# Performance work log

Hardware: AMD Instinct MI355X
Metric: run time of the kernel (lower is better)

## Reference

```python
import jax, jax.numpy as jnp
from jax import lax
import numpy as np

DN = ('NCHW', 'OIHW', 'NCHW')


def conv(x, w, b, pad=0):
    y = lax.conv_general_dilated(x, w, (1, 1), [(pad, pad), (pad, pad)],
                                 dimension_numbers=DN)
    return y + b[None, :, None, None]


def deconv(x, w, b, stride=1):
    # PyTorch ConvTranspose2d weight is (in, out, kH, kW); equivalent conv uses
    # flipped, in/out-transposed kernel with lhs dilation = stride, pad = k-1.
    k = w.shape[2]
    wt = jnp.flip(w, (2, 3)).transpose(1, 0, 2, 3)
    y = lax.conv_general_dilated(x, wt, (1, 1), [(k - 1, k - 1), (k - 1, k - 1)],
                                 lhs_dilation=(stride, stride), dimension_numbers=DN)
    return y + b[None, :, None, None]


def maxpool2(x):
    return lax.reduce_window(x, -jnp.inf, lax.max, (1, 1, 2, 2), (1, 1, 2, 2), 'VALID')


def setup_inputs() -> dict:
    key = jax.random.key(0)
    ks = jax.random.split(key, 12)
    B = 256

    def he(k, shape, fan_in):
        return jax.random.normal(k, shape, jnp.float32) * np.sqrt(2.0 / fan_in)

    inp = {
        'x': jax.random.normal(ks[0], (B, 1, 28, 28), jnp.float32),
        # encoder convs
        'w1': he(ks[1], (128, 1, 5, 5), 1 * 25), 'b1': jnp.zeros((128,), jnp.float32),
        'w2': he(ks[2], (128, 128, 5, 5), 128 * 25), 'b2': jnp.zeros((128,), jnp.float32),
        'w3': he(ks[3], (128, 128, 5, 5), 128 * 25), 'b3': jnp.zeros((128,), jnp.float32),
        # decoder transposed convs (torch shape: in, out, kH, kW)
        't1w': he(ks[4], (128, 128, 4, 4), 128 * 16), 't1b': jnp.zeros((128,), jnp.float32),
        't2w': he(ks[5], (128, 128, 4, 4), 128 * 16), 't2b': jnp.zeros((128,), jnp.float32),
        't3w': he(ks[6], (128, 128, 5, 5), 128 * 25), 't3b': jnp.zeros((128,), jnp.float32),
        't4w': he(ks[7], (128, 128, 5, 5), 128 * 25), 't4b': jnp.zeros((128,), jnp.float32),
        # mu_net 1x1 conv
        'mw': he(ks[8], (1, 128, 1, 1), 128), 'mb': jnp.zeros((1,), jnp.float32),
        # codebook: Embedding(128, 128), init ~ N(0, 1)
        'dict_w': jax.random.normal(ks[9], (128, 128), jnp.float32),
    }
    return inp


def reference(x, w1, b1, w2, b2, w3, b3,
              t1w, t1b, t2w, t2b, t3w, t3b, t4w, t4b,
              mw, mb, dict_w):
    BETA, RATE = 0.25, 5.0
    # ---- encoder ----
    h = jax.nn.relu(conv(x, w1, b1, pad=0))          # (B,128,24,24)
    h = jax.nn.relu(conv(h, w2, b2, pad=2))          # (B,128,24,24)
    h = maxpool2(h)                                  # (B,128,12,12)
    h = conv(h, w3, b3, pad=2)                       # (B,128,12,12)
    z = maxpool2(h)                                  # (B,128,6,6)

    # ---- nearest_neighbor (faithful: argmax of distance, as in the source) ----
    z_sg = lax.stop_gradient(z)
    z2 = jnp.sum(z_sg * z_sg, axis=1, keepdims=True)          # (B,1,6,6)
    w2n = jnp.sum(dict_w * dict_w, axis=1)                     # (K,)
    cross = jnp.einsum('bchw,kc->bkhw', z_sg, lax.stop_gradient(dict_w))
    d2 = z2 + w2n[None, :, None, None] - 2.0 * cross           # (B,K,6,6)
    index = jnp.argmax(d2, axis=1)                             # (B,6,6) int

    # ---- embedding gather ----
    val = dict_w[index].transpose(0, 3, 1, 2)                  # (B,128,6,6)

    # ---- decoder on detached codes ----
    f = lax.stop_gradient(val)
    f = jax.nn.relu(deconv(f, t1w, t1b, stride=1))             # (B,128,9,9)
    f = jax.nn.relu(deconv(f, t2w, t2b, stride=2))             # (B,128,20,20)
    f = jax.nn.relu(deconv(f, t3w, t3b, stride=1))             # (B,128,24,24)
    f = jax.nn.relu(deconv(f, t4w, t4b, stride=1))             # (B,128,28,28)
    mu = conv(f, mw, mb, pad=0)                                # (B,1,28,28)

    loss_rec = jnp.mean((mu - x) ** 2)
    dict_loss = jnp.mean((val - lax.stop_gradient(z)) ** 2) * RATE
    enc_loss = jnp.mean((z - lax.stop_gradient(val)) ** 2) * BETA * RATE
    var_loss = jnp.zeros((), jnp.float32)
    losses = jnp.stack([loss_rec, dict_loss, enc_loss, var_loss])
    return losses, index
```

## Files before the change

### kernel.cpp

```cpp
#include <hip/hip_runtime.h>
#include <hip/hip_bf16.h>


#define B_ 256

typedef __attribute__((ext_vector_type(8))) short s16x8;
typedef __attribute__((ext_vector_type(4))) short s16x4;
typedef __attribute__((ext_vector_type(8))) _Float16 f16x8;
typedef __attribute__((ext_vector_type(4))) float f32x4;

__device__ inline ushort f2bf(float f) {
  union { __hip_bfloat16 h; ushort u; } cv;
  cv.h = __float2bfloat16(f);
  return cv.u;
}

__global__ __launch_bounds__(256) void prep_all(
    const float* __restrict__ t1w, const float* __restrict__ t3w,
    const float* __restrict__ t4w, const float* __restrict__ t2w,
    const float* __restrict__ w2, const float* __restrict__ w3,
    ushort* __restrict__ wp1, ushort* __restrict__ wp3,
    ushort* __restrict__ wp4, ushort* __restrict__ wp2,
    _Float16* __restrict__ w2h, _Float16* __restrict__ w2l,
    _Float16* __restrict__ w3h, _Float16* __restrict__ w3l) {
  const int b = blockIdx.x, t = threadIdx.x;
  if (b < 1024) {
    int idx = b * 256 + t;
    int ci = idx & 127, co = (idx >> 7) & 127, tap = idx >> 14;
    wp1[idx] = f2bf(t1w[((size_t)ci * 128 + co) * 16 + (15 - tap)]);
  } else if (b < 2624) {
    int idx = (b - 1024) * 256 + t;
    int ci = idx & 127, co = (idx >> 7) & 127, tap = idx >> 14;
    wp3[idx] = f2bf(t3w[((size_t)ci * 128 + co) * 25 + (24 - tap)]);
  } else if (b < 4224) {
    int idx = (b - 2624) * 256 + t;
    int ci = idx & 127, co = (idx >> 7) & 127, tap = idx >> 14;
    wp4[idx] = f2bf(t4w[((size_t)ci * 128 + co) * 25 + (24 - tap)]);
  } else if (b < 5248) {
    int idx = (b - 4224) * 256 + t;
    int ci = idx & 127, co = (idx >> 7) & 127;
    int tap = (idx >> 14) & 3, pp = idx >> 16;
    int u = tap >> 1, v = tap & 1, py = pp >> 1, px = pp & 1;
    wp2[idx] = f2bf(
        t2w[(((size_t)ci * 128 + co) * 4 + (py + 2 * u)) * 4 + (px + 2 * v)]);
  } else if (b < 6848) {
    int idx = (b - 5248) * 256 + t;
    int ci = idx & 127, co = (idx >> 7) & 127, tap = idx >> 14;
    float v = w2[((size_t)co * 128 + ci) * 25 + tap];
    _Float16 h = (_Float16)v;
    w2h[idx] = h;
    w2l[idx] = (_Float16)(v - (float)h);
  } else {
    int idx = (b - 6848) * 256 + t;
    int ci = idx & 127, co = (idx >> 7) & 127, tap = idx >> 14;
    float v = w3[((size_t)co * 128 + ci) * 25 + tap];
    _Float16 h = (_Float16)v;
    w3h[idx] = h;
    w3l[idx] = (_Float16)(v - (float)h);
  }
}

__global__ __launch_bounds__(256) void conv1_kernel(
    const float* __restrict__ x, const float* __restrict__ w,
    const float* __restrict__ b, _Float16* __restrict__ oh,
    _Float16* __restrict__ ol) {
  const int n = blockIdx.x;
  __shared__ float xl[784];
  __shared__ float wl[128 * 25];
  __shared__ float bl[128];
  const int t = threadIdx.x;
  for (int e = t; e < 784; e += 256) xl[e] = x[n * 784 + e];
  for (int e = t; e < 3200; e += 256) wl[e] = w[e];
  if (t < 128) bl[t] = b[t];
  __syncthreads();
  const size_t nb = (size_t)n * 73728;
  for (int idx = t; idx < 73728; idx += 256) {
    int co = idx & 127, p = idx >> 7;
    int y = p / 24, xx = p % 24;
    float acc = bl[co];
    const float* wc = &wl[co * 25];
#pragma unroll
    for (int ky = 0; ky < 5; ky++)
#pragma unroll
      for (int kx = 0; kx < 5; kx++)
        acc += xl[(y + ky) * 28 + xx + kx] * wc[ky * 5 + kx];
    float v = fmaxf(acc, 0.f);
    _Float16 h = (_Float16)v;
    oh[nb + idx] = h;
    ol[nb + idx] = (_Float16)(v - (float)h);
  }
}

template <int IW, int K, int PAD, int TR, bool RELU, bool OUT_F32>
__global__ __launch_bounds__(256, 3) void conv_mfma_pool(
    const _Float16* __restrict__ inh, const _Float16* __restrict__ inl,
    const _Float16* __restrict__ wph, const _Float16* __restrict__ wpl,
    const float* __restrict__ bias, _Float16* __restrict__ outh,
    _Float16* __restrict__ outl, float* __restrict__ outf) {
  constexpr int IH = IW, OW = IW, OH = IW;
  constexpr int PW = IW + 2 * PAD;
  constexpr int SROWS = TR + K - 1;
  constexpr int S = SROWS * PW;
  constexpr int NPOS = TR * OW;
  constexpr int NCH = NPOS / 16;
  constexpr int K2 = K * K;
  constexpr int PITCH = 40;
  constexpr int LIN_ELT = S * PITCH;
  constexpr int LIN_BYTES = 2 * LIN_ELT * 2;
  constexpr int SCR_BYTES = 64 * NPOS * 4;
  constexpr int SMEM_BYTES = LIN_BYTES > SCR_BYTES ? LIN_BYTES : SCR_BYTES;
  static_assert(NPOS % 16 == 0, "");
  static_assert(TR % 2 == 0 && OW % 2 == 0, "");
  __shared__ __align__(16) char smem[SMEM_BYTES];
  _Float16* linh = (_Float16*)smem;
  _Float16* linl = linh + LIN_ELT;
  const int n = blockIdx.x;
  const int r0 = blockIdx.y * TR;
  const int t = threadIdx.x;
  const int wv = t >> 6;
  const int lane = t & 63;
  const int nn = lane & 15;
  const int q = lane >> 4;
  f32x4 acc0[NCH], acc1[NCH];
#pragma unroll
  for (int c = 0; c < NCH; c++) {
    acc0[c] = f32x4{0.f, 0.f, 0.f, 0.f};
    acc1[c] = f32x4{0.f, 0.f, 0.f, 0.f};
  }
  int base[NCH];
#pragma unroll
  for (int c = 0; c < NCH; c++) {
    int p = c * 16 + nn;
    base[c] = (p / OW) * PW + (p % OW);
  }
  const int rowA = wv * 16 + nn;
  const int rowB = (wv + 4) * 16 + nn;
  for (int cb = 0; cb < 4; cb++) {
    const int ci0 = cb * 32;
    __syncthreads();
    for (int e = t; e < S * 4; e += 256) {
      int sp = e >> 2, j = e & 3;
      int r = sp / PW, c = sp - r * PW;
      int ir = r0 + r - PAD, ic = c - PAD;
      f16x8 vh = {0, 0, 0, 0, 0, 0, 0, 0};
      f16x8 vl = {0, 0, 0, 0, 0, 0, 0, 0};
      if (ir >= 0 && ir < IH && ic >= 0 && ic < IW) {
        size_t g = ((size_t)n * (IH * IW) + ir * IW + ic) * 128 + ci0 + j * 8;
        vh = *(const f16x8*)&inh[g];
        vl = *(const f16x8*)&inl[g];
      }
      int st = sp * PITCH + ((j + (sp >> 3)) & 3) * 8;
      *(f16x8*)&linh[st] = vh;
      *(f16x8*)&linl[st] = vl;
    }
    __syncthreads();
    const size_t gA = (size_t)rowA * 128 + ci0 + q * 8;
    const size_t gB = (size_t)rowB * 128 + ci0 + q * 8;
    f16x8 cah0 = *(const f16x8*)&wph[gA];
    f16x8 cal0 = *(const f16x8*)&wpl[gA];
    f16x8 cah1 = *(const f16x8*)&wph[gB];
    f16x8 cal1 = *(const f16x8*)&wpl[gB];
    for (int tap = 0; tap < K2; tap++) {
      f16x8 nah0 = cah0, nal0 = cal0, nah1 = cah1, nal1 = cal1;
      if (tap + 1 < K2) {
        size_t oA = gA + (size_t)(tap + 1) * 16384;
        size_t oB = gB + (size_t)(tap + 1) * 16384;
        nah0 = *(const f16x8*)&wph[oA];
        nal0 = *(const f16x8*)&wpl[oA];
        nah1 = *(const f16x8*)&wph[oB];
        nal1 = *(const f16x8*)&wpl[oB];
      }
      const int ky = tap / K, kx = tap - ky * K;
      const int toff = ky * PW + kx;
#pragma unroll
      for (int c = 0; c < NCH; c++) {
        int s = base[c] + toff;
        int off = s * PITCH + ((q + (s >> 3)) & 3) * 8;
        f16x8 bh = *(const f16x8*)&linh[off];
        f16x8 bl = *(const f16x8*)&linl[off];
        acc0[c] =
            __builtin_amdgcn_mfma_f32_16x16x32_f16(cah0, bh, acc0[c], 0, 0, 0);
        acc0[c] =
            __builtin_amdgcn_mfma_f32_16x16x32_f16(cah0, bl, acc0[c], 0, 0, 0);
        acc0[c] =
            __builtin_amdgcn_mfma_f32_16x16x32_f16(cal0, bh, acc0[c], 0, 0, 0);
        acc1[c] =
            __builtin_amdgcn_mfma_f32_16x16x32_f16(cah1, bh, acc1[c], 0, 0, 0);
        acc1[c] =
            __builtin_amdgcn_mfma_f32_16x16x32_f16(cah1, bl, acc1[c], 0, 0, 0);
        acc1[c] =
            __builtin_amdgcn_mfma_f32_16x16x32_f16(cal1, bh, acc1[c], 0, 0, 0);
      }
      cah0 = nah0; cal0 = nal0; cah1 = nah1; cal1 = nal1;
    }
  }
  __syncthreads();
  float* scr = (float*)smem + wv * 16 * NPOS;
#pragma unroll
  for (int j = 0; j < 2; j++) {
    const int cot = (j ? wv + 4 : wv) * 16;
#pragma unroll
    for (int c = 0; c < NCH; c++) {
      f32x4 a = j ? acc1[c] : acc0[c];
#pragma unroll
      for (int r = 0; r < 4; r++) {
        float v = a[r] + bias[cot + q * 4 + r];
        if (RELU) v = fmaxf(v, 0.f);
        scr[(q * 4 + r) * NPOS + c * 16 + nn] = v;
      }
    }
    __syncthreads();
    for (int e = lane; e < 16 * (TR / 2) * (OW / 2); e += 64) {
      int co_l = e & 15;
      int rem = e >> 4;
      int pr = rem / (OW / 2), pc = rem - pr * (OW / 2);
      const float* s = scr + co_l * NPOS;
      int lp = (2 * pr) * OW + 2 * pc;
      float m =
          fmaxf(fmaxf(s[lp], s[lp + 1]), fmaxf(s[lp + OW], s[lp + OW + 1]));
      int sp_out = (r0 / 2 + pr) * (OW / 2) + pc;
      size_t go =
          ((size_t)n * ((OH / 2) * (OW / 2)) + sp_out) * 128 + cot + co_l;
      if (OUT_F32) {
        outf[go] = m;
      } else {
        _Float16 h = (_Float16)m;
        outh[go] = h;
        outl[go] = (_Float16)(m - (float)h);
      }
    }
    __syncthreads();
  }
}

__global__ __launch_bounds__(256) void vq_kernel(
    const float* __restrict__ z, const float* __restrict__ dict,
    float* __restrict__ val, ushort* __restrict__ val_bf,
    float* __restrict__ out_idx) {
  const int n = blockIdx.x;
  __shared__ float zl[36 * 128];
  __shared__ float d2[36 * 129];
  __shared__ float w2n[128];
  __shared__ int bk[36];
  const int t = threadIdx.x;
  const float* zn = z + (size_t)n * 4608;
  for (int e = t; e < 4608; e += 256) zl[e] = zn[e];
  if (t < 128) {
    float s = 0.f;
    const float* wr = dict + t * 128;
    for (int c = 0; c < 128; c++) s += wr[c] * wr[c];
    w2n[t] = s;
  }
  __syncthreads();
  const int k = t & 127, pg = t >> 7;
  float dot[18];
#pragma unroll
  for (int i = 0; i < 18; i++) dot[i] = 0.f;
  const float* wr = dict + k * 128;
  for (int c = 0; c < 128; c++) {
    float wv = wr[c];
#pragma unroll
    for (int i = 0; i < 18; i++) dot[i] += zl[(pg * 18 + i) * 128 + c] * wv;
  }
  float wn = w2n[k];
#pragma unroll
  for (int i = 0; i < 18; i++) d2[(pg * 18 + i) * 129 + k] = wn - 2.f * dot[i];
  __syncthreads();
  if (t < 36) {
    const float* dr = &d2[t * 129];
    float best = dr[0];
    int bi = 0;
    for (int kk = 1; kk < 128; kk++) {
      float v = dr[kk];
      if (v > best) { best = v; bi = kk; }
    }
    bk[t] = bi;
    out_idx[n * 36 + t] = (float)bi;
  }
  __syncthreads();
  float* vn = val + (size_t)n * 4608;
  ushort* vbn = val_bf + (size_t)n * 4608;
  for (int e = t; e < 4608; e += 256) {
    int c = e & 127, p = e >> 7;
    float v = dict[bk[p] * 128 + c];
    vn[e] = v;
    vbn[e] = f2bf(v);
  }
}

template <int IH, int IW, int OH, int OW, int K, int TR, bool MU_FUSE>
__global__ __launch_bounds__(256, 2) void deconv_mfma(
    const ushort* __restrict__ in, const ushort* __restrict__ wprep,
    const float* __restrict__ bias, const float* __restrict__ mw,
    void* __restrict__ outp) {
  constexpr int PAD = K - 1;
  constexpr int PW = IW + 2 * PAD;
  constexpr int K2 = K * K;
  constexpr int SROWS = TR + K - 1;
  constexpr int S = SROWS * PW;
  constexpr int NPOS = TR * OW;
  constexpr int NCH = (NPOS + 15) / 16;
  constexpr int PITCH = 40;
  constexpr int LIN_ELT = S * PITCH;
  constexpr int NSTG = (S * 4 + 255) / 256;
  __shared__ __align__(16) ushort lin[2][LIN_ELT];
  const int n = blockIdx.x;
  const int r0 = blockIdx.y * TR;
  const int t = threadIdx.x;
  const int wv = t >> 6;
  const int lane = t & 63;
  const int nn = lane & 15;
  const int q = lane >> 4;
  f32x4 acc0[NCH], acc1[NCH];
  int base[NCH];
#pragma unroll
  for (int c = 0; c < NCH; c++) {
    acc0[c] = f32x4{0.f, 0.f, 0.f, 0.f};
    acc1[c] = f32x4{0.f, 0.f, 0.f, 0.f};
    int p = c * 16 + nn;
    int pc = p < NPOS ? p : NPOS - 1;
    base[c] = (pc / OW) * PW + (pc % OW);
  }
  s16x8 stg[NSTG];
  auto load_stage = [&](int ci0) {
#pragma unroll
    for (int i = 0; i < NSTG; i++) {
      int e = t + i * 256;
      s16x8 v = {0, 0, 0, 0, 0, 0, 0, 0};
      if (e < S * 4) {
        int sp = e >> 2, j = e & 3;
        int rr = sp / PW, cc = sp - rr * PW;
        int ir = r0 + rr - PAD, ic = cc - PAD;
        if (ir >= 0 && ir < IH && ic >= 0 && ic < IW)
          v = *(const s16x8*)&in[((size_t)n * (IH * IW) + ir * IW + ic) * 128 +
                                 ci0 + j * 8];
      }
      stg[i] = v;
    }
  };
  auto store_stage = [&](int bsel) {
#pragma unroll
    for (int i = 0; i < NSTG; i++) {
      int e = t + i * 256;
      if (e < S * 4) {
        int sp = e >> 2, j = e & 3;
        *(s16x8*)&lin[bsel][sp * PITCH + ((j + (sp >> 3)) & 3) * 8] = stg[i];
      }
    }
  };

  load_stage(0);
  store_stage(0);
  __syncthreads();
  for (int cb = 0; cb < 4; cb++) {
    const int ci0 = cb * 32;
    if (cb < 3) load_stage(ci0 + 32);
    const ushort* L = lin[cb & 1];
    const size_t gA = (size_t)(wv * 16 + nn) * 128 + ci0 + q * 8;
    const size_t gB = (size_t)((wv + 4) * 16 + nn) * 128 + ci0 + q * 8;
    s16x8 ca0 = *(const s16x8*)&wprep[gA];
    s16x8 ca1 = *(const s16x8*)&wprep[gB];
    for (int tap = 0; tap < K2; tap++) {
      s16x8 na0 = ca0, na1 = ca1;
      if (tap + 1 < K2) {
        na0 = *(const s16x8*)&wprep[gA + (size_t)(tap + 1) * 16384];
        na1 = *(const s16x8*)&wprep[gB + (size_t)(tap + 1) * 16384];
      }
      const int ky = tap / K, kx = tap - ky * K;
      const int toff = ky * PW + kx;
#pragma unroll
      for (int c = 0; c < NCH; c++) {
        int s = base[c] + toff;
        s16x8 b = *(const s16x8*)&L[s * PITCH + ((q + (s >> 3)) & 3) * 8];
        acc0[c] =
            __builtin_amdgcn_mfma_f32_16x16x32_bf16(ca0, b, acc0[c], 0, 0, 0);
        acc1[c] =
            __builtin_amdgcn_mfma_f32_16x16x32_bf16(ca1, b, acc1[c], 0, 0, 0);
      }
      ca0 = na0; ca1 = na1;
    }
    if (cb < 3) {
      store_stage((cb + 1) & 1);
      __syncthreads();
    }
  }
  const int co_a = wv * 16 + q * 4;
  const int co_b = (wv + 4) * 16 + q * 4;
  float ba[4], bb[4];
#pragma unroll
  for (int r = 0; r < 4; r++) {
    ba[r] = bias[co_a + r];
    bb[r] = bias[co_b + r];
  }
  if (!MU_FUSE) {
    ushort* out = (ushort*)outp;
#pragma unroll
    for (int c = 0; c < NCH; c++) {
      int p = c * 16 + nn;
      if (p < NPOS) {
        size_t go = ((size_t)n * (OH * OW) + r0 * OW + p) * 128;
        s16x4 pa, pb;
#pragma unroll
        for (int r = 0; r < 4; r++) {
          pa[r] = (short)f2bf(fmaxf(acc0[c][r] + ba[r], 0.f));
          pb[r] = (short)f2bf(fmaxf(acc1[c][r] + bb[r], 0.f));
        }
        *(s16x4*)&out[go + co_a] = pa;
        *(s16x4*)&out[go + co_b] = pb;
      }
    }
  } else {
    float* out = (float*)outp;
    float wa[4], wb[4];
#pragma unroll
    for (int r = 0; r < 4; r++) {
      wa[r] = mw[co_a + r];
      wb[r] = mw[co_b + r];
    }
#pragma unroll
    for (int c = 0; c < NCH; c++) {
      int p = c * 16 + nn;
      float s = 0.f;
#pragma unroll
      for (int r = 0; r < 4; r++) {
        s += fmaxf(acc0[c][r] + ba[r], 0.f) * wa[r];
        s += fmaxf(acc1[c][r] + bb[r], 0.f) * wb[r];
      }
      s += __shfl_xor(s, 16);
      s += __shfl_xor(s, 32);
      if (q == 0 && p < NPOS)
        atomicAdd(&out[(size_t)n * (OH * OW) + r0 * OW + p], s);
    }
  }
}

__global__ __launch_bounds__(256, 3) void deconv_s2_mfma(
    const ushort* __restrict__ in, const ushort* __restrict__ wp2,
    const float* __restrict__ bias, ushort* __restrict__ out) {
  constexpr int NCH = 7;
  constexpr int PITCH = 40;
  const int n = blockIdx.x;
  const int pp = blockIdx.y;
  const int py = pp >> 1, px = pp & 1;
  __shared__ __align__(16) ushort lin[121 * PITCH];
  const int t = threadIdx.x;
  const int wv = t >> 6;
  const int lane = t & 63;
  const int nn = lane & 15;
  const int q = lane >> 4;
  f32x4 acc0[NCH], acc1[NCH];
  int base[NCH];
#pragma unroll
  for (int c = 0; c < NCH; c++) {
    acc0[c] = f32x4{0.f, 0.f, 0.f, 0.f};
    acc1[c] = f32x4{0.f, 0.f, 0.f, 0.f};
    int p = c * 16 + nn;
    int pc = p < 100 ? p : 99;
    base[c] = (pc / 10) * 11 + (pc % 10);
  }
  const int toffs[4] = {12, 11, 1, 0};
  for (int cb = 0; cb < 4; cb++) {
    const int ci0 = cb * 32;
    __syncthreads();
    for (int e = t; e < 121 * 4; e += 256) {
      int sp = e >> 2, j = e & 3;
      int r = sp / 11, c2 = sp - r * 11;
      int ir = r - 1, ic = c2 - 1;
      s16x8 v = {0, 0, 0, 0, 0, 0, 0, 0};
      if (ir >= 0 && ir < 9 && ic >= 0 && ic < 9)
        v = *(const s16x8*)&in[((size_t)n * 81 + ir * 9 + ic) * 128 + ci0 +
                               j * 8];
      *(s16x8*)&lin[sp * PITCH + ((j + (sp >> 3)) & 3) * 8] = v;
    }
    __syncthreads();
    const size_t gA =
        ((size_t)(pp * 4) * 128 + wv * 16 + nn) * 128 + ci0 + q * 8;
    const size_t gB =
        ((size_t)(pp * 4) * 128 + (wv + 4) * 16 + nn) * 128 + ci0 + q * 8;
    s16x8 ca0 = *(const s16x8*)&wp2[gA];
    s16x8 ca1 = *(const s16x8*)&wp2[gB];
    for (int tap = 0; tap < 4; tap++) {
      s16x8 na0 = ca0, na1 = ca1;
      if (tap + 1 < 4) {
        na0 = *(const s16x8*)&wp2[gA + (size_t)(tap + 1) * 16384];
        na1 = *(const s16x8*)&wp2[gB + (size_t)(tap + 1) * 16384];
      }
      const int toff = toffs[tap];
#pragma unroll
      for (int c = 0; c < NCH; c++) {
        int s = base[c] + toff;
        s16x8 b = *(const s16x8*)&lin[s * PITCH + ((q + (s >> 3)) & 3) * 8];
        acc0[c] =
            __builtin_amdgcn_mfma_f32_16x16x32_bf16(ca0, b, acc0[c], 0, 0, 0);
        acc1[c] =
            __builtin_amdgcn_mfma_f32_16x16x32_bf16(ca1, b, acc1[c], 0, 0, 0);
      }
      ca0 = na0; ca1 = na1;
    }
  }
  const int co_a = wv * 16 + q * 4;
  const int co_b = (wv + 4) * 16 + q * 4;
#pragma unroll
  for (int c = 0; c < NCH; c++) {
    int p = c * 16 + nn;
    if (p < 100) {
      int oy = 2 * (p / 10) + py, ox = 2 * (p % 10) + px;
      size_t go = ((size_t)n * 400 + oy * 20 + ox) * 128;
      s16x4 pa, pb;
#pragma unroll
      for (int r = 0; r < 4; r++) {
        pa[r] = (short)f2bf(fmaxf(acc0[c][r] + bias[co_a + r], 0.f));
        pb[r] = (short)f2bf(fmaxf(acc1[c][r] + bias[co_b + r], 0.f));
      }
      *(s16x4*)&out[go + co_a] = pa;
      *(s16x4*)&out[go + co_b] = pb;
    }
  }
}

__global__ __launch_bounds__(256) void loss_kernel(
    const float* __restrict__ mu, const float* __restrict__ mb,
    const float* __restrict__ x, const float4* __restrict__ val4,
    const float4* __restrict__ z4, float* __restrict__ out) {
  const int b = blockIdx.x, t = threadIdx.x;
  __shared__ float red[256];
  if (b < 784) {
    int i = b * 256 + t;
    float d = mu[i] + mb[0] - x[i];
    red[t] = d * d;
  } else {
    int i = (b - 784) * 256 + t;
    float4 a = val4[i], zz = z4[i];
    float dx = a.x - zz.x, dy = a.y - zz.y, dz = a.z - zz.z, dw = a.w - zz.w;
    red[t] = dx * dx + dy * dy + dz * dz + dw * dw;
  }
  __syncthreads();
  for (int off = 128; off > 0; off >>= 1) {
    if (t < off) red[t] += red[t + off];
    __syncthreads();
  }
  if (t == 0) {
    if (b < 784) {
      atomicAdd(out, red[0] * (1.0f / 200704.f));
    } else {
      atomicAdd(out + 1, red[0] * (5.f / 1179648.f));
      atomicAdd(out + 2, red[0] * (1.25f / 1179648.f));
    }
  }
}

extern "C" void kernel_launch(void* const* d_in, const int* in_sizes, int n_in,
                              void* d_out, int out_size, void* d_ws,
                              size_t ws_size, hipStream_t stream) {
  const float* x = (const float*)d_in[0];
  const float* w1 = (const float*)d_in[1];
  const float* b1 = (const float*)d_in[2];
  const float* w2 = (const float*)d_in[3];
  const float* b2 = (const float*)d_in[4];
  const float* w3 = (const float*)d_in[5];
  const float* b3 = (const float*)d_in[6];
  const float* t1w = (const float*)d_in[7];
  const float* t1b = (const float*)d_in[8];
  const float* t2w = (const float*)d_in[9];
  const float* t2b = (const float*)d_in[10];
  const float* t3w = (const float*)d_in[11];
  const float* t3b = (const float*)d_in[12];
  const float* t4w = (const float*)d_in[13];
  const float* t4b = (const float*)d_in[14];
  const float* mw = (const float*)d_in[15];
  const float* mb = (const float*)d_in[16];
  const float* dictw = (const float*)d_in[17];
  float* out = (float*)d_out;

  float* p = (float*)d_ws;
  _Float16* h1h = (_Float16*)p; p += 9437184;
  _Float16* h1l = (_Float16*)p; p += 9437184;
  _Float16* p1h = (_Float16*)p; p += 2359296;
  _Float16* p1l = (_Float16*)p; p += 2359296;
  float* z = p; p += 1179648;
  float* val = p; p += 1179648;
  ushort* val_bf = (ushort*)p; p += 589824;
  float* mu = p; p += 200704;
  ushort* wp1 = (ushort*)p; p += 131072;
  ushort* wp3 = (ushort*)p; p += 204800;
  ushort* wp4 = (ushort*)p; p += 204800;
  ushort* wp2 = (ushort*)p; p += 131072;
  _Float16* w2h = (_Float16*)p; p += 204800;
  _Float16* w2l = (_Float16*)p; p += 204800;
  _Float16* w3h = (_Float16*)p; p += 204800;
  _Float16* w3l = (_Float16*)p; p += 204800;
  ushort* f1 = (ushort*)p1h;
  ushort* f2 = (ushort*)h1l;
  ushort* f3 = (ushort*)h1h;

  hipMemsetAsync(d_out, 0, 4 * sizeof(float), stream);
  hipMemsetAsync(mu, 0, 200704 * sizeof(float), stream);

  prep_all<<<8448, 256, 0, stream>>>(t1w, t3w, t4w, t2w, w2, w3, wp1, wp3, wp4,
                                     wp2, w2h, w2l, w3h, w3l);

  conv1_kernel<<<B_, 256, 0, stream>>>(x, w1, b1, h1h, h1l);
  conv_mfma_pool<24, 5, 2, 6, true, false>
      <<<dim3(B_, 4), 256, 0, stream>>>(h1h, h1l, w2h, w2l, b2, p1h, p1l,
                                        nullptr);
  conv_mfma_pool<12, 5, 2, 4, false, true>
      <<<dim3(B_, 3), 256, 0, stream>>>(p1h, p1l, w3h, w3l, b3, nullptr,
                                        nullptr, z);
  vq_kernel<<<B_, 256, 0, stream>>>(z, dictw, val, val_bf, out + 4);
  deconv_mfma<6, 6, 9, 9, 4, 9, false>
      <<<dim3(B_, 1), 256, 0, stream>>>(val_bf, wp1, t1b, nullptr, f1);
  deconv_s2_mfma<<<dim3(B_, 4), 256, 0, stream>>>(f1, wp2, t2b, f2);
  deconv_mfma<20, 20, 24, 24, 5, 8, false>
      <<<dim3(B_, 3), 256, 0, stream>>>(f2, wp3, t3b, nullptr, f3);
  deconv_mfma<24, 24, 28, 28, 5, 7, true>
      <<<dim3(B_, 4), 256, 0, stream>>>(f3, wp4, t4b, mw, mu);
  loss_kernel<<<1936, 256, 0, stream>>>(mu, mb, x, (const float4*)val,
                                        (const float4*)z, out);
}
```

Baseline: 957.0 us.

## Split deconv work by spatial position across waves, each wave covering all channels

Adds a deconv_mfma_ps kernel for the last two transposed convolutions. Each wave now owns a subset of output-position chunks and all 128 output channels (8 MFMA tiles), where previously each wave owned 32 output channels across all positions. Each LDS activation fragment is therefore reused across 8 weight tiles, at the cost of loading 8 weight fragments per tap from global memory and holding more accumulators, which raises register pressure (launch bounds 256,2). In the fused mu stage each output pixel is now produced by a single wave, so the atomicAdd and the mu memset are replaced by a plain store.

Measured after the change: 1.330 ms. 38.9% more time.

```diff
diff --git a/kernel.cpp b/kernel.cpp
--- a/kernel.cpp
+++ b/kernel.cpp
@@ -392,44 +392,126 @@
     ba[r] = bias[co_a + r];
     bb[r] = bias[co_b + r];
   }
+  ushort* out = (ushort*)outp;
+#pragma unroll
+  for (int c = 0; c < NCH; c++) {
+    int p = c * 16 + nn;
+    if (p < NPOS) {
+      size_t go = ((size_t)n * (OH * OW) + r0 * OW + p) * 128;
+      s16x4 pa, pb;
+#pragma unroll
+      for (int r = 0; r < 4; r++) {
+        pa[r] = (short)f2bf(fmaxf(acc0[c][r] + ba[r], 0.f));
+        pb[r] = (short)f2bf(fmaxf(acc1[c][r] + bb[r], 0.f));
+      }
+      *(s16x4*)&out[go + co_a] = pa;
+      *(s16x4*)&out[go + co_b] = pb;
+    }
+  }
+}
+
+template <int IH, int IW, int OH, int OW, int K, int TR, bool MU_FUSE>
+__global__ __launch_bounds__(256, 2) void deconv_mfma_ps(
+    const ushort* __restrict__ in, const ushort* __restrict__ wprep,
+    const float* __restrict__ bias, const float* __restrict__ mw,
+    void* __restrict__ outp) {
+  constexpr int PAD = K - 1;
+  constexpr int PW = IW + 2 * PAD;
+  constexpr int K2 = K * K;
+  constexpr int SROWS = TR + K - 1;
+  constexpr int S = SROWS * PW;
+  constexpr int NPOS = TR * OW;
+  constexpr int NCH = (NPOS + 15) / 16;
+  constexpr int MAXC = (NCH + 3) / 4;
+  constexpr int PITCH = 40;
+  __shared__ __align__(16) ushort lin[S * PITCH];
+  const int n = blockIdx.x;
+  const int r0 = blockIdx.y * TR;
+  const int t = threadIdx.x;
+  const int wv = t >> 6;
+  const int lane = t & 63;
+  const int nn = lane & 15;
+  const int q = lane >> 4;
+  f32x4 acc[8][MAXC];
+#pragma unroll
+  for (int j = 0; j < 8; j++)
+#pragma unroll
+    for (int k = 0; k < MAXC; k++) acc[j][k] = f32x4{0.f, 0.f, 0.f, 0.f};
+  int base[MAXC];
+#pragma unroll
+  for (int k = 0; k < MAXC; k++) {
+    int cidx = wv + 4 * k;
+    int p = cidx * 16 + nn;
+    int pc = p < NPOS ? p : NPOS - 1;
+    base[k] = (pc / OW) * PW + (pc % OW);
+  }
+  for (int cb = 0; cb < 4; cb++) {
+    const int ci0 = cb * 32;
+    __syncthreads();
+    for (int e = t; e < S * 4; e += 256) {
+      int sp = e >> 2, j = e & 3;
+      int rr = sp / PW, cc = sp - rr * PW;
+      int ir = r0 + rr - PAD, ic = cc - PAD;
+      s16x8 v = {0, 0, 0, 0, 0, 0, 0, 0};
+      if (ir >= 0 && ir < IH && ic >= 0 && ic < IW)
+        v = *(const s16x8*)&in[((size_t)n * (IH * IW) + ir * IW + ic) * 128 +
+                               ci0 + j * 8];
+      *(s16x8*)&lin[sp * PITCH + ((j + (sp >> 3)) & 3) * 8] = v;
+    }
+    __syncthreads();
+    const size_t abase = (size_t)nn * 128 + ci0 + q * 8;
+    for (int tap = 0; tap < K2; tap++) {
+      const size_t tb = (size_t)tap * 16384 + abase;
+      s16x8 a[8];
+#pragma unroll
+      for (int j = 0; j < 8; j++)
+        a[j] = *(const s16x8*)&wprep[tb + (size_t)j * 2048];
+      const int ky = tap / K, kx = tap - ky * K;
+      const int toff = ky * PW + kx;
+#pragma unroll
+      for (int k = 0; k < MAXC; k++) {
+        int s = base[k] + toff;
+        s16x8 b = *(const s16x8*)&lin[s * PITCH + ((q + (s >> 3)) & 3) * 8];
+#pragma unroll
+        for (int j = 0; j < 8; j++)
+          acc[j][k] =
+              __builtin_amdgcn_mfma_f32_16x16x32_bf16(a[j], b, acc[j][k], 0, 0, 0);
+      }
+    }
+  }
   if (!MU_FUSE) {
     ushort* out = (ushort*)outp;
 #pragma unroll
-    for (int c = 0; c < NCH; c++) {
-      int p = c * 16 + nn;
+    for (int k = 0; k < MAXC; k++) {
+      int p = (wv + 4 * k) * 16 + nn;
       if (p < NPOS) {
-        size_t go = ((size_t)n * (OH * OW) + r0 * OW + p) * 128;
-        s16x4 pa, pb;
-#pragma unroll
-        for (int r = 0; r < 4; r++) {
-          pa[r] = (short)f2bf(fmaxf(acc0[c][r] + ba[r], 0.f));
-          pb[r] = (short)f2bf(fmaxf(acc1[c][r] + bb[r], 0.f));
+        size_t go = ((size_t)n * (OH * OW) + r0 * OW + p) * 128 + q * 4;
+#pragma unroll
+        for (int j = 0; j < 8; j++) {
+          s16x4 pk;
+#pragma unroll
+          for (int r = 0; r < 4; r++)
+            pk[r] = (short)f2bf(fmaxf(acc[j][k][r] + bias[j * 16 + q * 4 + r], 0.f));
+          *(s16x4*)&out[go + j * 16] = pk;
         }
-        *(s16x4*)&out[go + co_a] = pa;
-        *(s16x4*)&out[go + co_b] = pb;
       }
     }
   } else {
     float* out = (float*)outp;
-    float wa[4], wb[4];
-#pragma unroll
-    for (int r = 0; r < 4; r++) {
-      wa[r] = mw[co_a + r];
-      wb[r] = mw[co_b + r];
-    }
-#pragma unroll
-    for (int c = 0; c < NCH; c++) {
-      int p = c * 16 + nn;
+#pragma unroll
+    for (int k = 0; k < MAXC; k++) {
+      int p = (wv + 4 * k) * 16 + nn;
       float s = 0.f;
 #pragma unroll
-      for (int r = 0; r < 4; r++) {
-        s += fmaxf(acc0[c][r] + ba[r], 0.f) * wa[r];
-        s += fmaxf(acc1[c][r] + bb[r], 0.f) * wb[r];
-      }
+      for (int j = 0; j < 8; j++)
+#pragma unroll
+        for (int r = 0; r < 4; r++) {
+          int co = j * 16 + q * 4 + r;
+          s += fmaxf(acc[j][k][r] + bias[co], 0.f) * mw[co];
+        }
       s += __shfl_xor(s, 16);
       s += __shfl_xor(s, 32);
-      if (q == 0 && p < NPOS)
-        atomicAdd(&out[(size_t)n * (OH * OW) + r0 * OW + p], s);
+      if (q == 0 && p < NPOS) out[(size_t)n * (OH * OW) + r0 * OW + p] = s;
     }
   }
 }
@@ -594,7 +676,6 @@
   ushort* f3 = (ushort*)h1h;
 
   hipMemsetAsync(d_out, 0, 4 * sizeof(float), stream);
-  hipMemsetAsync(mu, 0, 200704 * sizeof(float), stream);
 
   prep_all<<<8448, 256, 0, stream>>>(t1w, t3w, t4w, t2w, w2, w3, wp1, wp3, wp4,
                                      wp2, w2h, w2l, w3h, w3l);
@@ -610,9 +691,9 @@
   deconv_mfma<6, 6, 9, 9, 4, 9, false>
       <<<dim3(B_, 1), 256, 0, stream>>>(val_bf, wp1, t1b, nullptr, f1);
   deconv_s2_mfma<<<dim3(B_, 4), 256, 0, stream>>>(f1, wp2, t2b, f2);
-  deconv_mfma<20, 20, 24, 24, 5, 8, false>
+  deconv_mfma_ps<20, 20, 24, 24, 5, 8, false>
       <<<dim3(B_, 3), 256, 0, stream>>>(f2, wp3, t3b, nullptr, f3);
-  deconv_mfma<24, 24, 28, 28, 5, 7, true>
+  deconv_mfma_ps<24, 24, 28, 28, 5, 7, true>
       <<<dim3(B_, 4), 256, 0, stream>>>(f3, wp4, t4b, mw, mu);
   loss_kernel<<<1936, 256, 0, stream>>>(mu, mb, x, (const float4*)val,
                                         (const float4*)z, out);
```
